# Optimization experiments

Measured on AMD Instinct MI355X. Metric: run time of the kernel, lower is better.

Reference implementation:

```python
import jax, jax.numpy as jnp
import numpy as np

B, QL, KVL, DQ, DKV = 8192, 24, 24, 12, 512


def setup_inputs() -> dict:
    key = jax.random.key(0)
    ks = jax.random.split(key, 9)
    s = lambda fan_in: 1.0 / np.sqrt(fan_in)
    return {
        "q": jax.random.normal(ks[0], (B, QL, DQ), jnp.float32),
        "k": jax.random.normal(ks[1], (B, KVL, DKV), jnp.float32),
        "v": jax.random.normal(ks[2], (B, KVL, DKV), jnp.float32),
        "Wq": jax.random.uniform(ks[3], (DQ, DQ), jnp.float32, -s(DQ), s(DQ)),
        "bq": jax.random.uniform(ks[4], (DQ,), jnp.float32, -s(DQ), s(DQ)),
        "Wk": jax.random.uniform(ks[5], (DQ, DKV), jnp.float32, -s(DKV), s(DKV)),
        "bk": jax.random.uniform(ks[6], (DQ,), jnp.float32, -s(DKV), s(DKV)),
        "Wl": jax.random.uniform(ks[7], (DQ, KVL), jnp.float32, -s(KVL), s(KVL)),
        "bl": jax.random.uniform(ks[8], (DQ,), jnp.float32, -s(KVL), s(KVL)),
    }


def reference(q, k, v, Wq, bq, Wk, bk, Wl, bl):
    # q: [b, q_len, dim_q], k: [b, kv_len, dim_kv]; v is unused (as in source).
    q_proj = jnp.einsum("bqd,ed->bqe", q, Wq) + bq          # [b, q_len, dim_q]
    k_proj = jnp.einsum("bkf,ef->bke", k, Wk) + bk          # [b, kv_len, dim_q]
    qk = jnp.einsum("bqe,bke->bqk", q_proj, k_proj)          # [b, q_len, kv_len]
    a_q = jax.nn.softmax(qk, axis=1)                         # softmax over q_len
    a_k = jax.nn.softmax(qk, axis=2)                         # softmax over kv_len
    c_q = jnp.einsum("bqk,bke->bqe", a_q, k_proj)            # [b, q_len, dim_q]
    qc = jnp.concatenate([q, c_q], axis=2)                   # [b, q_len, 2*dim_q]
    c_k = jnp.einsum("bqk,bqe->bke", a_k, qc)                # [b, kv_len, 2*dim_q]
    # linear over kv_len (== seq_len) dim: c_k^T [b, 2*dim_q, kv_len] -> [b, 2*dim_q, dim_q]
    attn = jnp.einsum("bke,dk->bed", c_k, Wl) + bl
    return attn
```

## Files before the change

kernel.cpp:

```cpp
#include <hip/hip_runtime.h>


#define DPP_ADD(x, ctrl, rmask)                                                   \
  x += __int_as_float(__builtin_amdgcn_update_dpp(                                \
      0, __float_as_int(x), ctrl, rmask, 0xF, false))

__device__ __forceinline__ float wave_sum64(float x) {
  DPP_ADD(x, 0xB1, 0xF);
  DPP_ADD(x, 0x4E, 0xF);
  DPP_ADD(x, 0x141, 0xF);
  DPP_ADD(x, 0x140, 0xF);
  DPP_ADD(x, 0x142, 0xA);
  DPP_ADD(x, 0x143, 0xC);
  return x;
}

#define DPP_BF(x, OP, ctrl)                                                       \
  {                                                                               \
    float _t = __int_as_float(__builtin_amdgcn_update_dpp(                        \
        0, __float_as_int(x), ctrl, 0xF, 0xF, true));                             \
    x = OP(x, _t);                                                                \
  }
__device__ __forceinline__ float bf32_max(float x) {
  DPP_BF(x, fmaxf, 0xB1);
  DPP_BF(x, fmaxf, 0x4E);
  DPP_BF(x, fmaxf, 0x141);
  DPP_BF(x, fmaxf, 0x140);
  float t = __int_as_float(__builtin_amdgcn_ds_swizzle(__float_as_int(x), 0x401F));
  return fmaxf(x, t);
}
__device__ __forceinline__ float bf32_add(float x) {
  DPP_ADD(x, 0xB1, 0xF);
  DPP_ADD(x, 0x4E, 0xF);
  DPP_ADD(x, 0x141, 0xF);
  DPP_ADD(x, 0x140, 0xF);
  float t = __int_as_float(__builtin_amdgcn_ds_swizzle(__float_as_int(x), 0x401F));
  return x + t;
}

__device__ __forceinline__ float dot12(const float* a, float4 b0, float4 b1, float4 b2) {
  return a[0] * b0.x + a[1] * b0.y + a[2] * b0.z + a[3] * b0.w +
         a[4] * b1.x + a[5] * b1.y + a[6] * b1.z + a[7] * b1.w +
         a[8] * b2.x + a[9] * b2.y + a[10] * b2.z + a[11] * b2.w;
}

__global__ __launch_bounds__(64) void coattn_kernel(
    const float* __restrict__ q, const float* __restrict__ k,
    const float* __restrict__ Wq, const float* __restrict__ bq,
    const float* __restrict__ Wk, const float* __restrict__ bk,
    const float* __restrict__ Wl, const float* __restrict__ bl,
    float* __restrict__ out) {
  constexpr int QL = 24, KVL = 24, DQ = 12, DKV = 512;

  __shared__ alignas(16) float kp[KVL][DQ];
  __shared__ alignas(16) float qc[QL][24];
  __shared__ alignas(16) float akT[KVL][28];
  __shared__ alignas(16) float ckL[KVL][28];
  __shared__ alignas(16) float WqL[DQ][DQ];
  __shared__ alignas(16) float WlT[KVL][DQ];
  __shared__ alignas(16) float bqL[DQ], bkL[DQ], blL[DQ];

  const int lane = threadIdx.x;
  const int b = blockIdx.x;
  const int li = (lane < 24) ? lane : 0;

  for (int p = lane; p < DQ * DQ; p += 64) WqL[p / DQ][p % DQ] = Wq[p];
  for (int p = lane; p < DQ * KVL; p += 64) WlT[p % KVL][p / KVL] = Wl[p];
  const float* qb = q + (size_t)b * (QL * DQ);
  for (int p = lane; p < QL * DQ; p += 64) qc[p / DQ][p % DQ] = qb[p];
  if (lane < DQ) {
    bqL[lane] = bq[lane];
    bkL[lane] = bk[lane];
    blL[lane] = bl[lane];
  }

  const float4* WkV = reinterpret_cast<const float4*>(Wk);
  float4 wk0[DQ], wk1[DQ];
#pragma unroll
  for (int e = 0; e < DQ; ++e) {
    wk0[e] = WkV[e * 128 + lane];
    wk1[e] = WkV[e * 128 + 64 + lane];
  }

  const float4* kbV = reinterpret_cast<const float4*>(k + (size_t)b * (KVL * DKV));

#define KROW(AC, BC, ROW)                                                          \
  {                                                                                \
    float pp[DQ];                                                                  \
    _Pragma("unroll") for (int e = 0; e < DQ; ++e) {                               \
      pp[e] = (AC).x * wk0[e].x + (AC).y * wk0[e].y + (AC).z * wk0[e].z +          \
              (AC).w * wk0[e].w + (BC).x * wk1[e].x + (BC).y * wk1[e].y +          \
              (BC).z * wk1[e].z + (BC).w * wk1[e].w;                               \
    }                                                                              \
    _Pragma("unroll") for (int e = 0; e < DQ; ++e) pp[e] = wave_sum64(pp[e]);      \
    if (lane == 63) {                                                              \
      float4 w0, w1, w2;                                                           \
      w0.x = pp[0]; w0.y = pp[1]; w0.z = pp[2]; w0.w = pp[3];                      \
      w1.x = pp[4]; w1.y = pp[5]; w1.z = pp[6]; w1.w = pp[7];                      \
      w2.x = pp[8]; w2.y = pp[9]; w2.z = pp[10]; w2.w = pp[11];                    \
      *(float4*)&kp[ROW][0] = w0;                                                  \
      *(float4*)&kp[ROW][4] = w1;                                                  \
      *(float4*)&kp[ROW][8] = w2;                                                  \
    }                                                                              \
  }

  float4 A0 = kbV[0 * 128 + lane], B0 = kbV[0 * 128 + 64 + lane];
  float4 A1 = kbV[1 * 128 + lane], B1 = kbV[1 * 128 + 64 + lane];
  float4 A2, B2, A3, B3;
  for (int kv = 0; kv < KVL; kv += 4) {
    {
      const int r = kv + 2;
      A2 = kbV[r * 128 + lane];
      B2 = kbV[r * 128 + 64 + lane];
    }
    KROW(A0, B0, kv);
    {
      const int r = kv + 3;
      A3 = kbV[r * 128 + lane];
      B3 = kbV[r * 128 + 64 + lane];
    }
    KROW(A1, B1, kv + 1);
    {
      const int r = (kv + 4 < KVL) ? kv + 4 : KVL - 1;
      A0 = kbV[r * 128 + lane];
      B0 = kbV[r * 128 + 64 + lane];
    }
    KROW(A2, B2, kv + 2);
    {
      const int r = (kv + 5 < KVL) ? kv + 5 : KVL - 1;
      A1 = kbV[r * 128 + lane];
      B1 = kbV[r * 128 + 64 + lane];
    }
    KROW(A3, B3, kv + 3);
  }
#undef KROW

  float qr[DQ];
  {
    float4 t0 = *(const float4*)&qc[li][0];
    float4 t1 = *(const float4*)&qc[li][4];
    float4 t2 = *(const float4*)&qc[li][8];
    qr[0] = t0.x; qr[1] = t0.y; qr[2] = t0.z; qr[3] = t0.w;
    qr[4] = t1.x; qr[5] = t1.y; qr[6] = t1.z; qr[7] = t1.w;
    qr[8] = t2.x; qr[9] = t2.y; qr[10] = t2.z; qr[11] = t2.w;
  }
  float bqr[DQ];
  {
    float4 t0 = *(const float4*)&bqL[0];
    float4 t1 = *(const float4*)&bqL[4];
    float4 t2 = *(const float4*)&bqL[8];
    bqr[0] = t0.x; bqr[1] = t0.y; bqr[2] = t0.z; bqr[3] = t0.w;
    bqr[4] = t1.x; bqr[5] = t1.y; bqr[6] = t1.z; bqr[7] = t1.w;
    bqr[8] = t2.x; bqr[9] = t2.y; bqr[10] = t2.z; bqr[11] = t2.w;
  }
  float qp_[DQ];
#pragma unroll
  for (int e = 0; e < DQ; ++e) {
    float4 w0 = *(const float4*)&WqL[e][0];
    float4 w1 = *(const float4*)&WqL[e][4];
    float4 w2 = *(const float4*)&WqL[e][8];
    qp_[e] = bqr[e] + dot12(qr, w0, w1, w2);
  }

  float bkr[DQ];
  {
    float4 t0 = *(const float4*)&bkL[0];
    float4 t1 = *(const float4*)&bkL[4];
    float4 t2 = *(const float4*)&bkL[8];
    bkr[0] = t0.x; bkr[1] = t0.y; bkr[2] = t0.z; bkr[3] = t0.w;
    bkr[4] = t1.x; bkr[5] = t1.y; bkr[6] = t1.z; bkr[7] = t1.w;
    bkr[8] = t2.x; bkr[9] = t2.y; bkr[10] = t2.z; bkr[11] = t2.w;
  }
  float qbk = 0.f;
#pragma unroll
  for (int e = 0; e < DQ; ++e) qbk += qp_[e] * bkr[e];

  float qkr[KVL];
#pragma unroll
  for (int kk = 0; kk < KVL; ++kk) {
    float4 k0 = *(const float4*)&kp[kk][0];
    float4 k1 = *(const float4*)&kp[kk][4];
    float4 k2 = *(const float4*)&kp[kk][8];
    qkr[kk] = qbk + dot12(qp_, k0, k1, k2);
  }
  if (lane >= 24 && lane < 32) {
#pragma unroll
    for (int j = 0; j < KVL; ++j) qkr[j] = -1e30f;
  }

  float akr[KVL];
  {
    float rm = qkr[0];
#pragma unroll
    for (int j = 1; j < KVL; ++j) rm = fmaxf(rm, qkr[j]);
    float s = 0.f;
#pragma unroll
    for (int j = 0; j < KVL; ++j) {
      akr[j] = __expf(qkr[j] - rm);
      s += akr[j];
    }
    const float inv = __builtin_amdgcn_rcpf(s);
#pragma unroll
    for (int j = 0; j < KVL; ++j) akr[j] *= inv;
  }

#pragma unroll
  for (int j = 0; j < KVL; ++j) {
    const float m = bf32_max(qkr[j]);
    const float t = __expf(qkr[j] - m);
    const float s2 = bf32_add(t);
    qkr[j] = t * __builtin_amdgcn_rcpf(s2);
  }

  float sa = 0.f;
#pragma unroll
  for (int j = 0; j < KVL; ++j) sa += qkr[j];
  float cq[DQ];
#pragma unroll
  for (int e = 0; e < DQ; ++e) cq[e] = bkr[e] * sa;
#pragma unroll
  for (int kk = 0; kk < KVL; ++kk) {
    float4 k0 = *(const float4*)&kp[kk][0];
    float4 k1 = *(const float4*)&kp[kk][4];
    float4 k2 = *(const float4*)&kp[kk][8];
    const float a = qkr[kk];
    cq[0] += a * k0.x; cq[1] += a * k0.y; cq[2] += a * k0.z; cq[3] += a * k0.w;
    cq[4] += a * k1.x; cq[5] += a * k1.y; cq[6] += a * k1.z; cq[7] += a * k1.w;
    cq[8] += a * k2.x; cq[9] += a * k2.y; cq[10] += a * k2.z; cq[11] += a * k2.w;
  }
  if (lane < 24) {
    float4 w0, w1, w2;
    w0.x = cq[0]; w0.y = cq[1]; w0.z = cq[2]; w0.w = cq[3];
    w1.x = cq[4]; w1.y = cq[5]; w1.z = cq[6]; w1.w = cq[7];
    w2.x = cq[8]; w2.y = cq[9]; w2.z = cq[10]; w2.w = cq[11];
    *(float4*)&qc[li][12] = w0;
    *(float4*)&qc[li][16] = w1;
    *(float4*)&qc[li][20] = w2;
#pragma unroll
    for (int kk = 0; kk < KVL; ++kk) akT[kk][li] = akr[kk];
  }

  float ak[QL];
  {
    float4 a0 = *(const float4*)&akT[li][0];
    float4 a1 = *(const float4*)&akT[li][4];
    float4 a2 = *(const float4*)&akT[li][8];
    float4 a3 = *(const float4*)&akT[li][12];
    float4 a4 = *(const float4*)&akT[li][16];
    float4 a5 = *(const float4*)&akT[li][20];
    ak[0] = a0.x; ak[1] = a0.y; ak[2] = a0.z; ak[3] = a0.w;
    ak[4] = a1.x; ak[5] = a1.y; ak[6] = a1.z; ak[7] = a1.w;
    ak[8] = a2.x; ak[9] = a2.y; ak[10] = a2.z; ak[11] = a2.w;
    ak[12] = a3.x; ak[13] = a3.y; ak[14] = a3.z; ak[15] = a3.w;
    ak[16] = a4.x; ak[17] = a4.y; ak[18] = a4.z; ak[19] = a4.w;
    ak[20] = a5.x; ak[21] = a5.y; ak[22] = a5.z; ak[23] = a5.w;
  }
  float ck[24];
#pragma unroll
  for (int e = 0; e < 24; ++e) ck[e] = 0.f;
#pragma unroll
  for (int qq = 0; qq < QL; ++qq) {
    float4 c0 = *(const float4*)&qc[qq][0];
    float4 c1 = *(const float4*)&qc[qq][4];
    float4 c2 = *(const float4*)&qc[qq][8];
    float4 c3 = *(const float4*)&qc[qq][12];
    float4 c4 = *(const float4*)&qc[qq][16];
    float4 c5 = *(const float4*)&qc[qq][20];
    const float a = ak[qq];
    ck[0] += a * c0.x; ck[1] += a * c0.y; ck[2] += a * c0.z; ck[3] += a * c0.w;
    ck[4] += a * c1.x; ck[5] += a * c1.y; ck[6] += a * c1.z; ck[7] += a * c1.w;
    ck[8] += a * c2.x; ck[9] += a * c2.y; ck[10] += a * c2.z; ck[11] += a * c2.w;
    ck[12] += a * c3.x; ck[13] += a * c3.y; ck[14] += a * c3.z; ck[15] += a * c3.w;
    ck[16] += a * c4.x; ck[17] += a * c4.y; ck[18] += a * c4.z; ck[19] += a * c4.w;
    ck[20] += a * c5.x; ck[21] += a * c5.y; ck[22] += a * c5.z; ck[23] += a * c5.w;
  }
  if (lane < 24) {
    float4 w0, w1, w2, w3, w4, w5;
    w0.x = ck[0]; w0.y = ck[1]; w0.z = ck[2]; w0.w = ck[3];
    w1.x = ck[4]; w1.y = ck[5]; w1.z = ck[6]; w1.w = ck[7];
    w2.x = ck[8]; w2.y = ck[9]; w2.z = ck[10]; w2.w = ck[11];
    w3.x = ck[12]; w3.y = ck[13]; w3.z = ck[14]; w3.w = ck[15];
    w4.x = ck[16]; w4.y = ck[17]; w4.z = ck[18]; w4.w = ck[19];
    w5.x = ck[20]; w5.y = ck[21]; w5.z = ck[22]; w5.w = ck[23];
    *(float4*)&ckL[li][0] = w0;
    *(float4*)&ckL[li][4] = w1;
    *(float4*)&ckL[li][8] = w2;
    *(float4*)&ckL[li][12] = w3;
    *(float4*)&ckL[li][16] = w4;
    *(float4*)&ckL[li][20] = w5;
  }

  float acc[DQ];
  {
    float4 t0 = *(const float4*)&blL[0];
    float4 t1 = *(const float4*)&blL[4];
    float4 t2 = *(const float4*)&blL[8];
    acc[0] = t0.x; acc[1] = t0.y; acc[2] = t0.z; acc[3] = t0.w;
    acc[4] = t1.x; acc[5] = t1.y; acc[6] = t1.z; acc[7] = t1.w;
    acc[8] = t2.x; acc[9] = t2.y; acc[10] = t2.z; acc[11] = t2.w;
  }
#pragma unroll
  for (int kk = 0; kk < KVL; ++kk) {
    const float cv = ckL[kk][li];
    float4 w0 = *(const float4*)&WlT[kk][0];
    float4 w1 = *(const float4*)&WlT[kk][4];
    float4 w2 = *(const float4*)&WlT[kk][8];
    acc[0] += cv * w0.x; acc[1] += cv * w0.y; acc[2] += cv * w0.z; acc[3] += cv * w0.w;
    acc[4] += cv * w1.x; acc[5] += cv * w1.y; acc[6] += cv * w1.z; acc[7] += cv * w1.w;
    acc[8] += cv * w2.x; acc[9] += cv * w2.y; acc[10] += cv * w2.z; acc[11] += cv * w2.w;
  }
  if (lane < 24) {
    float* ob = out + (size_t)b * 288 + li * 12;
    float4 w0, w1, w2;
    w0.x = acc[0]; w0.y = acc[1]; w0.z = acc[2]; w0.w = acc[3];
    w1.x = acc[4]; w1.y = acc[5]; w1.z = acc[6]; w1.w = acc[7];
    w2.x = acc[8]; w2.y = acc[9]; w2.z = acc[10]; w2.w = acc[11];
    *(float4*)(ob + 0) = w0;
    *(float4*)(ob + 4) = w1;
    *(float4*)(ob + 8) = w2;
  }
}

extern "C" void kernel_launch(void* const* d_in, const int* in_sizes, int n_in,
                              void* d_out, int out_size, void* d_ws, size_t ws_size,
                              hipStream_t stream) {
  const float* q = (const float*)d_in[0];
  const float* k = (const float*)d_in[1];
  const float* Wq = (const float*)d_in[3];
  const float* bq = (const float*)d_in[4];
  const float* Wk = (const float*)d_in[5];
  const float* bk = (const float*)d_in[6];
  const float* Wl = (const float*)d_in[7];
  const float* bl = (const float*)d_in[8];
  float* out = (float*)d_out;

  const int B = in_sizes[0] / (24 * 12);
  coattn_kernel<<<B, 64, 0, stream>>>(q, k, Wq, bq, Wk, bk, Wl, bl, out);
}
```

Measured before the change: 129.4 us.

## Split K projection into separate MFMA kernel using bf16x3 split precision

Moves the dominant k×Wk projection (512-wide reduction per row) out of the per-batch fused kernel into a dedicated kernel. That kernel runs bf16 MFMA instructions, splitting each fp32 value into hi and lo bf16 halves with three products to keep near-fp32 accuracy. The projected keys go through a workspace buffer to a second kernel that does the small attention tail. The aim is to put the bandwidth- and FMA-heavy projection on matrix cores with better occupancy, at the cost of an extra launch and a workspace round trip. The old fused kernel is kept as a fallback.

```diff
diff --git a/kernel.cpp b/kernel.cpp
--- a/kernel.cpp
+++ b/kernel.cpp
@@ -1,5 +1,93 @@
 #include <hip/hip_runtime.h>
 
+
+typedef short s16x8 __attribute__((ext_vector_type(8)));
+typedef float f32x4 __attribute__((ext_vector_type(4)));
+
+__global__ __launch_bounds__(512, 6) void kproj_mfma(
+    const float* __restrict__ k, const float* __restrict__ Wk,
+    float* __restrict__ kp) {
+  constexpr int WPAD = 520;
+  __shared__ short lwk_hi[12 * WPAD];
+  __shared__ short lwk_lo[12 * WPAD];
+
+  const int tid = threadIdx.x;
+
+  for (int i = tid; i < 12 * 512; i += 512) {
+    const int e = i >> 9, d = i & 511;
+    const float f = Wk[i];
+    const unsigned u = __float_as_uint(f);
+    const unsigned hib = u & 0xFFFF0000u;
+    const float lo = f - __uint_as_float(hib);
+    lwk_hi[e * WPAD + d] = (short)(u >> 16);
+    lwk_lo[e * WPAD + d] = (short)(__float_as_uint(lo) >> 16);
+  }
+  __syncthreads();
+
+  const int wave = tid >> 6;
+  const int lane = tid & 63;
+  const int rowL = lane & 15;
+  const int kgrp = lane >> 4;
+  const int e_eff = (rowL < 12) ? rowL : 11;
+
+  const int r0 = blockIdx.x * 256 + wave * 16;
+  const int r1 = r0 + 128;
+
+  const short* bhi_base = &lwk_hi[e_eff * WPAD];
+  const short* blo_base = &lwk_lo[e_eff * WPAD];
+  const float* a0base = k + (size_t)(r0 + rowL) * 512 + kgrp * 8;
+  const float* a1base = k + (size_t)(r1 + rowL) * 512 + kgrp * 8;
+
+  f32x4 acc0 = {0.f, 0.f, 0.f, 0.f};
+  f32x4 acc1 = {0.f, 0.f, 0.f, 0.f};
+
+#pragma unroll 2
+  for (int s = 0; s < 16; ++s) {
+    const int kb = s * 32 + kgrp * 8;
+    float4 x0 = *(const float4*)(a0base + s * 32);
+    float4 x1 = *(const float4*)(a0base + s * 32 + 4);
+    float4 y0 = *(const float4*)(a1base + s * 32);
+    float4 y1 = *(const float4*)(a1base + s * 32 + 4);
+    s16x8 bhi = *(const s16x8*)(bhi_base + kb);
+    s16x8 blo = *(const s16x8*)(blo_base + kb);
+
+    s16x8 ahi0, alo0, ahi1, alo1;
+    {
+      const float fx[8] = {x0.x, x0.y, x0.z, x0.w, x1.x, x1.y, x1.z, x1.w};
+      const float fy[8] = {y0.x, y0.y, y0.z, y0.w, y1.x, y1.y, y1.z, y1.w};
+#pragma unroll
+      for (int j = 0; j < 8; ++j) {
+        unsigned ux = __float_as_uint(fx[j]);
+        unsigned hx = ux & 0xFFFF0000u;
+        float lx = fx[j] - __uint_as_float(hx);
+        ahi0[j] = (short)(ux >> 16);
+        alo0[j] = (short)(__float_as_uint(lx) >> 16);
+        unsigned uy = __float_as_uint(fy[j]);
+        unsigned hy = uy & 0xFFFF0000u;
+        float ly = fy[j] - __uint_as_float(hy);
+        ahi1[j] = (short)(uy >> 16);
+        alo1[j] = (short)(__float_as_uint(ly) >> 16);
+      }
+    }
+
+    acc0 = __builtin_amdgcn_mfma_f32_16x16x32_bf16(ahi0, bhi, acc0, 0, 0, 0);
+    acc1 = __builtin_amdgcn_mfma_f32_16x16x32_bf16(ahi1, bhi, acc1, 0, 0, 0);
+    acc0 = __builtin_amdgcn_mfma_f32_16x16x32_bf16(ahi0, blo, acc0, 0, 0, 0);
+    acc1 = __builtin_amdgcn_mfma_f32_16x16x32_bf16(ahi1, blo, acc1, 0, 0, 0);
+    acc0 = __builtin_amdgcn_mfma_f32_16x16x32_bf16(alo0, bhi, acc0, 0, 0, 0);
+    acc1 = __builtin_amdgcn_mfma_f32_16x16x32_bf16(alo1, bhi, acc1, 0, 0, 0);
+  }
+
+  if (rowL < 12) {
+    float* o0 = kp + (size_t)(r0 + kgrp * 4) * 12 + rowL;
+    float* o1 = kp + (size_t)(r1 + kgrp * 4) * 12 + rowL;
+#pragma unroll
+    for (int i = 0; i < 4; ++i) {
+      o0[i * 12] = acc0[i];
+      o1[i * 12] = acc1[i];
+    }
+  }
+}
 
 #define DPP_ADD(x, ctrl, rmask)                                                   \
   x += __int_as_float(__builtin_amdgcn_update_dpp(                                \
@@ -42,6 +130,225 @@
   return a[0] * b0.x + a[1] * b0.y + a[2] * b0.z + a[3] * b0.w +
          a[4] * b1.x + a[5] * b1.y + a[6] * b1.z + a[7] * b1.w +
          a[8] * b2.x + a[9] * b2.y + a[10] * b2.z + a[11] * b2.w;
+}
+
+__global__ __launch_bounds__(64) void coattn_tail(
+    const float* __restrict__ q, const float* __restrict__ kpg,
+    const float* __restrict__ Wq, const float* __restrict__ bq,
+    const float* __restrict__ bk,
+    const float* __restrict__ Wl, const float* __restrict__ bl,
+    float* __restrict__ out) {
+  constexpr int QL = 24, KVL = 24, DQ = 12;
+
+  __shared__ alignas(16) float kp[KVL][DQ];
+  __shared__ alignas(16) float qc[QL][24];
+  __shared__ alignas(16) float akT[KVL][28];
+  __shared__ alignas(16) float ckL[KVL][28];
+  __shared__ alignas(16) float WqL[DQ][DQ];
+  __shared__ alignas(16) float WlT[KVL][DQ];
+  __shared__ alignas(16) float bqL[DQ], bkL[DQ], blL[DQ];
+
+  const int lane = threadIdx.x;
+  const int b = blockIdx.x;
+  const int li = (lane < 24) ? lane : 0;
+
+  for (int p = lane; p < DQ * DQ; p += 64) WqL[p / DQ][p % DQ] = Wq[p];
+  for (int p = lane; p < DQ * KVL; p += 64) WlT[p % KVL][p / KVL] = Wl[p];
+  const float* qb = q + (size_t)b * (QL * DQ);
+  for (int p = lane; p < QL * DQ; p += 64) qc[p / DQ][p % DQ] = qb[p];
+  const float4* kpV = reinterpret_cast<const float4*>(kpg + (size_t)b * 288);
+  float* kpf = &kp[0][0];
+  for (int p = lane; p < 72; p += 64) *(float4*)&kpf[p * 4] = kpV[p];
+  if (lane < DQ) {
+    bqL[lane] = bq[lane];
+    bkL[lane] = bk[lane];
+    blL[lane] = bl[lane];
+  }
+
+  float qr[DQ];
+  {
+    float4 t0 = *(const float4*)&qc[li][0];
+    float4 t1 = *(const float4*)&qc[li][4];
+    float4 t2 = *(const float4*)&qc[li][8];
+    qr[0] = t0.x; qr[1] = t0.y; qr[2] = t0.z; qr[3] = t0.w;
+    qr[4] = t1.x; qr[5] = t1.y; qr[6] = t1.z; qr[7] = t1.w;
+    qr[8] = t2.x; qr[9] = t2.y; qr[10] = t2.z; qr[11] = t2.w;
+  }
+  float bqr[DQ];
+  {
+    float4 t0 = *(const float4*)&bqL[0];
+    float4 t1 = *(const float4*)&bqL[4];
+    float4 t2 = *(const float4*)&bqL[8];
+    bqr[0] = t0.x; bqr[1] = t0.y; bqr[2] = t0.z; bqr[3] = t0.w;
+    bqr[4] = t1.x; bqr[5] = t1.y; bqr[6] = t1.z; bqr[7] = t1.w;
+    bqr[8] = t2.x; bqr[9] = t2.y; bqr[10] = t2.z; bqr[11] = t2.w;
+  }
+  float qp_[DQ];
+#pragma unroll
+  for (int e = 0; e < DQ; ++e) {
+    float4 w0 = *(const float4*)&WqL[e][0];
+    float4 w1 = *(const float4*)&WqL[e][4];
+    float4 w2 = *(const float4*)&WqL[e][8];
+    qp_[e] = bqr[e] + dot12(qr, w0, w1, w2);
+  }
+
+  float bkr[DQ];
+  {
+    float4 t0 = *(const float4*)&bkL[0];
+    float4 t1 = *(const float4*)&bkL[4];
+    float4 t2 = *(const float4*)&bkL[8];
+    bkr[0] = t0.x; bkr[1] = t0.y; bkr[2] = t0.z; bkr[3] = t0.w;
+    bkr[4] = t1.x; bkr[5] = t1.y; bkr[6] = t1.z; bkr[7] = t1.w;
+    bkr[8] = t2.x; bkr[9] = t2.y; bkr[10] = t2.z; bkr[11] = t2.w;
+  }
+  float qbk = 0.f;
+#pragma unroll
+  for (int e = 0; e < DQ; ++e) qbk += qp_[e] * bkr[e];
+
+  float qkr[KVL];
+#pragma unroll
+  for (int kk = 0; kk < KVL; ++kk) {
+    float4 k0 = *(const float4*)&kp[kk][0];
+    float4 k1 = *(const float4*)&kp[kk][4];
+    float4 k2 = *(const float4*)&kp[kk][8];
+    qkr[kk] = qbk + dot12(qp_, k0, k1, k2);
+  }
+  if (lane >= 24 && lane < 32) {
+#pragma unroll
+    for (int j = 0; j < KVL; ++j) qkr[j] = -1e30f;
+  }
+
+  float akr[KVL];
+  {
+    float rm = qkr[0];
+#pragma unroll
+    for (int j = 1; j < KVL; ++j) rm = fmaxf(rm, qkr[j]);
+    float s = 0.f;
+#pragma unroll
+    for (int j = 0; j < KVL; ++j) {
+      akr[j] = __expf(qkr[j] - rm);
+      s += akr[j];
+    }
+    const float inv = __builtin_amdgcn_rcpf(s);
+#pragma unroll
+    for (int j = 0; j < KVL; ++j) akr[j] *= inv;
+  }
+
+#pragma unroll
+  for (int j = 0; j < KVL; ++j) {
+    const float m = bf32_max(qkr[j]);
+    const float t = __expf(qkr[j] - m);
+    const float s2 = bf32_add(t);
+    qkr[j] = t * __builtin_amdgcn_rcpf(s2);
+  }
+
+  float sa = 0.f;
+#pragma unroll
+  for (int j = 0; j < KVL; ++j) sa += qkr[j];
+  float cq[DQ];
+#pragma unroll
+  for (int e = 0; e < DQ; ++e) cq[e] = bkr[e] * sa;
+#pragma unroll
+  for (int kk = 0; kk < KVL; ++kk) {
+    float4 k0 = *(const float4*)&kp[kk][0];
+    float4 k1 = *(const float4*)&kp[kk][4];
+    float4 k2 = *(const float4*)&kp[kk][8];
+    const float a = qkr[kk];
+    cq[0] += a * k0.x; cq[1] += a * k0.y; cq[2] += a * k0.z; cq[3] += a * k0.w;
+    cq[4] += a * k1.x; cq[5] += a * k1.y; cq[6] += a * k1.z; cq[7] += a * k1.w;
+    cq[8] += a * k2.x; cq[9] += a * k2.y; cq[10] += a * k2.z; cq[11] += a * k2.w;
+  }
+  if (lane < 24) {
+    float4 w0, w1, w2;
+    w0.x = cq[0]; w0.y = cq[1]; w0.z = cq[2]; w0.w = cq[3];
+    w1.x = cq[4]; w1.y = cq[5]; w1.z = cq[6]; w1.w = cq[7];
+    w2.x = cq[8]; w2.y = cq[9]; w2.z = cq[10]; w2.w = cq[11];
+    *(float4*)&qc[li][12] = w0;
+    *(float4*)&qc[li][16] = w1;
+    *(float4*)&qc[li][20] = w2;
+#pragma unroll
+    for (int kk = 0; kk < KVL; ++kk) akT[kk][li] = akr[kk];
+  }
+
+  float ak[QL];
+  {
+    float4 a0 = *(const float4*)&akT[li][0];
+    float4 a1 = *(const float4*)&akT[li][4];
+    float4 a2 = *(const float4*)&akT[li][8];
+    float4 a3 = *(const float4*)&akT[li][12];
+    float4 a4 = *(const float4*)&akT[li][16];
+    float4 a5 = *(const float4*)&akT[li][20];
+    ak[0] = a0.x; ak[1] = a0.y; ak[2] = a0.z; ak[3] = a0.w;
+    ak[4] = a1.x; ak[5] = a1.y; ak[6] = a1.z; ak[7] = a1.w;
+    ak[8] = a2.x; ak[9] = a2.y; ak[10] = a2.z; ak[11] = a2.w;
+    ak[12] = a3.x; ak[13] = a3.y; ak[14] = a3.z; ak[15] = a3.w;
+    ak[16] = a4.x; ak[17] = a4.y; ak[18] = a4.z; ak[19] = a4.w;
+    ak[20] = a5.x; ak[21] = a5.y; ak[22] = a5.z; ak[23] = a5.w;
+  }
+  float ck[24];
+#pragma unroll
+  for (int e = 0; e < 24; ++e) ck[e] = 0.f;
+#pragma unroll
+  for (int qq = 0; qq < QL; ++qq) {
+    float4 c0 = *(const float4*)&qc[qq][0];
+    float4 c1 = *(const float4*)&qc[qq][4];
+    float4 c2 = *(const float4*)&qc[qq][8];
+    float4 c3 = *(const float4*)&qc[qq][12];
+    float4 c4 = *(const float4*)&qc[qq][16];
+    float4 c5 = *(const float4*)&qc[qq][20];
+    const float a = ak[qq];
+    ck[0] += a * c0.x; ck[1] += a * c0.y; ck[2] += a * c0.z; ck[3] += a * c0.w;
+    ck[4] += a * c1.x; ck[5] += a * c1.y; ck[6] += a * c1.z; ck[7] += a * c1.w;
+    ck[8] += a * c2.x; ck[9] += a * c2.y; ck[10] += a * c2.z; ck[11] += a * c2.w;
+    ck[12] += a * c3.x; ck[13] += a * c3.y; ck[14] += a * c3.z; ck[15] += a * c3.w;
+    ck[16] += a * c4.x; ck[17] += a * c4.y; ck[18] += a * c4.z; ck[19] += a * c4.w;
+    ck[20] += a * c5.x; ck[21] += a * c5.y; ck[22] += a * c5.z; ck[23] += a * c5.w;
+  }
+  if (lane < 24) {
+    float4 w0, w1, w2, w3, w4, w5;
+    w0.x = ck[0]; w0.y = ck[1]; w0.z = ck[2]; w0.w = ck[3];
+    w1.x = ck[4]; w1.y = ck[5]; w1.z = ck[6]; w1.w = ck[7];
+    w2.x = ck[8]; w2.y = ck[9]; w2.z = ck[10]; w2.w = ck[11];
+    w3.x = ck[12]; w3.y = ck[13]; w3.z = ck[14]; w3.w = ck[15];
+    w4.x = ck[16]; w4.y = ck[17]; w4.z = ck[18]; w4.w = ck[19];
+    w5.x = ck[20]; w5.y = ck[21]; w5.z = ck[22]; w5.w = ck[23];
+    *(float4*)&ckL[li][0] = w0;
+    *(float4*)&ckL[li][4] = w1;
+    *(float4*)&ckL[li][8] = w2;
+    *(float4*)&ckL[li][12] = w3;
+    *(float4*)&ckL[li][16] = w4;
+    *(float4*)&ckL[li][20] = w5;
+  }
+
+  float acc[DQ];
+  {
+    float4 t0 = *(const float4*)&blL[0];
+    float4 t1 = *(const float4*)&blL[4];
+    float4 t2 = *(const float4*)&blL[8];
+    acc[0] = t0.x; acc[1] = t0.y; acc[2] = t0.z; acc[3] = t0.w;
+    acc[4] = t1.x; acc[5] = t1.y; acc[6] = t1.z; acc[7] = t1.w;
+    acc[8] = t2.x; acc[9] = t2.y; acc[10] = t2.z; acc[11] = t2.w;
+  }
+#pragma unroll
+  for (int kk = 0; kk < KVL; ++kk) {
+    const float cv = ckL[kk][li];
+    float4 w0 = *(const float4*)&WlT[kk][0];
+    float4 w1 = *(const float4*)&WlT[kk][4];
+    float4 w2 = *(const float4*)&WlT[kk][8];
+    acc[0] += cv * w0.x; acc[1] += cv * w0.y; acc[2] += cv * w0.z; acc[3] += cv * w0.w;
+    acc[4] += cv * w1.x; acc[5] += cv * w1.y; acc[6] += cv * w1.z; acc[7] += cv * w1.w;
+    acc[8] += cv * w2.x; acc[9] += cv * w2.y; acc[10] += cv * w2.z; acc[11] += cv * w2.w;
+  }
+  if (lane < 24) {
+    float* ob = out + (size_t)b * 288 + li * 12;
+    float4 w0, w1, w2;
+    w0.x = acc[0]; w0.y = acc[1]; w0.z = acc[2]; w0.w = acc[3];
+    w1.x = acc[4]; w1.y = acc[5]; w1.z = acc[6]; w1.w = acc[7];
+    w2.x = acc[8]; w2.y = acc[9]; w2.z = acc[10]; w2.w = acc[11];
+    *(float4*)(ob + 0) = w0;
+    *(float4*)(ob + 4) = w1;
+    *(float4*)(ob + 8) = w2;
+  }
 }
 
 __global__ __launch_bounds__(64) void coattn_kernel(
@@ -335,5 +642,14 @@
   float* out = (float*)d_out;
 
   const int B = in_sizes[0] / (24 * 12);
-  coattn_kernel<<<B, 64, 0, stream>>>(q, k, Wq, bq, Wk, bk, Wl, bl, out);
-}
+  const int rows = B * 24;
+  const size_t kp_bytes = (size_t)rows * 12 * sizeof(float);
+
+  if (ws_size >= kp_bytes && (rows % 256) == 0) {
+    float* kp = (float*)d_ws;
+    kproj_mfma<<<rows / 256, 512, 0, stream>>>(k, Wk, kp);
+    coattn_tail<<<B, 64, 0, stream>>>(q, kp, Wq, bq, bk, Wl, bl, out);
+  } else {
+    coattn_kernel<<<B, 64, 0, stream>>>(q, k, Wq, bq, Wk, bk, Wl, bl, out);
+  }
+}
```

After: 154.4 us. 19.3% more time.
